# Performance work log

Measured on AMD Instinct MI355X. Metric: run time of the kernel, lower is better.

Reference implementation:

```python
import jax, jax.numpy as jnp
import numpy as np

NUM_BITS = 10
MEM_SIZE = 2 ** NUM_BITS  # 1024
HIDDEN = 1024
INPUT = 1024
BATCH = 16384
LN_EPS = 1e-5


def setup_inputs() -> dict:
    key = jax.random.key(0)
    ks = jax.random.split(key, 8)
    s = 0.02
    return {
        "x": jax.random.normal(ks[0], (BATCH, INPUT), jnp.float32),
        "h_prev": jax.random.normal(ks[1], (BATCH, HIDDEN), jnp.float32),
        "memory": jax.random.normal(ks[2], (MEM_SIZE, HIDDEN), jnp.float32),
        "W_w": jax.random.normal(ks[3], (HIDDEN, INPUT), jnp.float32) * s,
        "W_b": jnp.zeros((HIDDEN,), jnp.float32),
        "U_w": jax.random.normal(ks[4], (HIDDEN, HIDDEN), jnp.float32) * s,
        "U_b": jnp.zeros((HIDDEN,), jnp.float32),
        "Q_w": jax.random.normal(ks[5], (HIDDEN, HIDDEN), jnp.float32) * s,
        "Q_b": jnp.zeros((HIDDEN,), jnp.float32),
        "M_w": jax.random.normal(ks[6], (NUM_BITS, HIDDEN), jnp.float32) * s,
        "M_b": jnp.zeros((NUM_BITS,), jnp.float32),
        "ln_g": jnp.ones((HIDDEN,), jnp.float32),
        "ln_b": jnp.zeros((HIDDEN,), jnp.float32),
    }


def reference(x, h_prev, memory, W_w, W_b, U_w, U_b, Q_w, Q_b, M_w, M_b, ln_g, ln_b):
    # Binary address from h_prev (eval-mode hard threshold, non-differentiable)
    powers = jnp.asarray(2 ** np.arange(NUM_BITS - 1, -1, -1), dtype=x.dtype)  # [num_bits]
    logits = h_prev @ M_w.T + M_b                              # [B, num_bits]
    binary = (jax.nn.sigmoid(logits) > 0.5).astype(x.dtype)    # hard bits
    index = jnp.clip((binary * powers).sum(-1).astype(jnp.int32), 0, MEM_SIZE - 1)  # [B]
    h_mem = memory[index]                                      # gather [B, H]
    # Fused linear combine + LayerNorm + sigmoid
    pre = x @ W_w.T + W_b + h_prev @ U_w.T + U_b + h_mem @ Q_w.T + Q_b  # [B, H]
    mu = pre.mean(-1, keepdims=True)
    var = ((pre - mu) ** 2).mean(-1, keepdims=True)            # biased var (torch LN)
    norm = (pre - mu) * jax.lax.rsqrt(var + LN_EPS)
    return jax.nn.sigmoid(norm * ln_g + ln_b)                  # h_new [B, H]
```

## Files before the change

### kernel.cpp

```cpp
#include <hip/hip_runtime.h>

#define BATCH   16384
#define HIDDEN  1024
#define K2      2048
#define MEMSZ   1024
#define NBITS   10

#define BM 256
#define BN 256
#define BK 64
#define NT (K2 / BK)

typedef __bf16 bf16x8 __attribute__((ext_vector_type(8)));
typedef float  f32x4  __attribute__((ext_vector_type(4)));

__device__ __forceinline__ unsigned short f2bf(float f) {
    unsigned int u = __float_as_uint(f);
    u += 0x7FFFu + ((u >> 16) & 1u);
    return (unsigned short)(u >> 16);
}

__device__ __forceinline__ void gload_lds16(const void* g, void* l) {
    __builtin_amdgcn_global_load_lds(
        (const __attribute__((address_space(1))) unsigned int*)g,
        (__attribute__((address_space(3))) unsigned int*)l,
        16, 0, 0);
}

__global__ __launch_bounds__(256) void pack_build_kernel(
        const float* __restrict__ W, const float* __restrict__ U,
        const float* __restrict__ memory, const float* __restrict__ Q,
        const float* __restrict__ x, const float* __restrict__ h_prev,
        const float* __restrict__ M_w, const float* __restrict__ M_b,
        unsigned short* __restrict__ Bm, unsigned short* __restrict__ Mem,
        unsigned short* __restrict__ Qb, unsigned short* __restrict__ A,
        int* __restrict__ idxbuf) {
    if (blockIdx.x < 4096) {
        int u = blockIdx.x * 256 + threadIdx.x;
        const float* src;
        unsigned short* dst;
        if (u < 524288) {
            int n = u >> 9;
            int k = (u & 511) * 4;
            src = (k < 1024) ? (W + (size_t)n * 1024 + k)
                             : (U + (size_t)n * 1024 + (k - 1024));
            dst = Bm + (size_t)n * K2 + k;
        } else if (u < 786432) {
            int f = (u - 524288) * 4;
            src = memory + f;  dst = Mem + f;
        } else {
            int f = (u - 786432) * 4;
            src = Q + f;  dst = Qb + f;
        }
        float4 v = *reinterpret_cast<const float4*>(src);
        ushort4 o;
        o.x = f2bf(v.x); o.y = f2bf(v.y); o.z = f2bf(v.z); o.w = f2bf(v.w);
        *reinterpret_cast<ushort4*>(dst) = o;
        return;
    }

    int row  = ((blockIdx.x - 4096) * 256 + threadIdx.x) >> 6;
    int lane = threadIdx.x & 63;
    if (row >= BATCH) return;

    const float4* hp = reinterpret_cast<const float4*>(h_prev + (size_t)row * HIDDEN);
    float4 hv[4];
#pragma unroll
    for (int i = 0; i < 4; ++i) hv[i] = hp[i * 64 + lane];

    int idx = 0;
#pragma unroll
    for (int j = 0; j < NBITS; ++j) {
        const float4* mp = reinterpret_cast<const float4*>(M_w + (size_t)j * HIDDEN);
        float s = 0.f;
#pragma unroll
        for (int i = 0; i < 4; ++i) {
            float4 m = mp[i * 64 + lane];
            s += hv[i].x * m.x + hv[i].y * m.y + hv[i].z * m.z + hv[i].w * m.w;
        }
#pragma unroll
        for (int off = 32; off >= 1; off >>= 1) s += __shfl_xor(s, off, 64);
        float logit = s + M_b[j];
        if (logit > 0.f) idx |= (1 << (NBITS - 1 - j));
    }
    if (lane == 0) idxbuf[row] = idx;

    unsigned short* arow = A + (size_t)row * K2;
    const float4* xp = reinterpret_cast<const float4*>(x + (size_t)row * HIDDEN);
#pragma unroll
    for (int i = 0; i < 4; ++i) {
        int off = i * 256 + lane * 4;
        float4 vx = xp[i * 64 + lane];
        ushort4 ox; ox.x = f2bf(vx.x); ox.y = f2bf(vx.y); ox.z = f2bf(vx.z); ox.w = f2bf(vx.w);
        *reinterpret_cast<ushort4*>(arow + off) = ox;

        ushort4 oh; oh.x = f2bf(hv[i].x); oh.y = f2bf(hv[i].y); oh.z = f2bf(hv[i].z); oh.w = f2bf(hv[i].w);
        *reinterpret_cast<ushort4*>(arow + 1024 + off) = oh;
    }
}

__global__ __launch_bounds__(256) void mq_kernel(
        const unsigned short* __restrict__ Mem,
        const unsigned short* __restrict__ Qb,
        float* __restrict__ MQ) {
    __shared__ unsigned short As[128 * 64];
    __shared__ unsigned short Bs[128 * 64];

    const int ks = blockIdx.x >> 6;
    const int mb = (blockIdx.x >> 3) & 7;
    const int nb = blockIdx.x & 7;
    const int t    = threadIdx.x;
    const int lane = t & 63;
    const int w    = t >> 6;
    const int wr   = w >> 1, wc = w & 1;
    const int rr   = lane & 15, rq = lane >> 4;
    const int c8   = (t & 7) * 8;
    const int srow = t >> 3;

    f32x4 acc[4][4] = {};

    for (int kt = 0; kt < 4; ++kt) {
        const int k0 = ks * 256 + kt * 64;
#pragma unroll
        for (int i = 0; i < 4; ++i) {
            int r = i * 32 + srow;
            gload_lds16(Mem + (size_t)(mb * 128 + r) * 1024 + k0 + c8, As + i * 2048 + t * 8);
            gload_lds16(Qb  + (size_t)(nb * 128 + r) * 1024 + k0 + c8, Bs + i * 2048 + t * 8);
        }
        __syncthreads();
#pragma unroll
        for (int kk = 0; kk < 2; ++kk) {
            const int krd = kk * 32 + rq * 8;
            bf16x8 af[4], bfv[4];
#pragma unroll
            for (int m = 0; m < 4; ++m)
                af[m] = *reinterpret_cast<const bf16x8*>(As + (wr * 64 + m * 16 + rr) * 64 + krd);
#pragma unroll
            for (int n = 0; n < 4; ++n)
                bfv[n] = *reinterpret_cast<const bf16x8*>(Bs + (wc * 64 + n * 16 + rr) * 64 + krd);
#pragma unroll
            for (int m = 0; m < 4; ++m)
#pragma unroll
                for (int n = 0; n < 4; ++n)
                    acc[m][n] = __builtin_amdgcn_mfma_f32_16x16x32_bf16(
                        af[m], bfv[n], acc[m][n], 0, 0, 0);
        }
        __syncthreads();
    }

#pragma unroll
    for (int m = 0; m < 4; ++m)
#pragma unroll
        for (int n = 0; n < 4; ++n) {
            int gcol = nb * 128 + wc * 64 + n * 16 + rr;
#pragma unroll
            for (int j = 0; j < 4; ++j) {
                int grow = mb * 128 + wr * 64 + m * 16 + rq * 4 + j;
                atomicAdd(&MQ[(size_t)grow * 1024 + gcol], acc[m][n][j]);
            }
        }
}


__device__ __forceinline__ void stage_g(const unsigned short* __restrict__ src,
                                        int rowbase, int kt, int g,
                                        unsigned short* ldsTile, int t) {
    const int o      = g * 8192 + t * 16;
    const int row    = o >> 7;
    const int inner  = o & 127;
    const int sinner = inner ^ ((row & 7) << 4);
    const char* gp = reinterpret_cast<const char*>(
                         src + (size_t)(rowbase + row) * K2 + kt * BK) + sinner;
    gload_lds16(gp, reinterpret_cast<char*>(ldsTile) + o);
}

__device__ __forceinline__ bf16x8 ldsfrag(const unsigned short* tile, int row,
                                          int kbyte_x_sw) {
    return *reinterpret_cast<const bf16x8*>(
        reinterpret_cast<const char*>(tile) + row * 128 + kbyte_x_sw);
}

#define WAIT_PH(N)                                                   \
    do {                                                             \
        asm volatile("" ::: "memory");                               \
        __builtin_amdgcn_s_barrier();                                \
        asm volatile("s_waitcnt lgkmcnt(" #N ")" ::: "memory");      \
        __builtin_amdgcn_sched_barrier(0);                           \
    } while (0)

#define BAR_OUT()                                                    \
    do {                                                             \
        __builtin_amdgcn_sched_barrier(0);                           \
        asm volatile("" ::: "memory");                               \
        __builtin_amdgcn_s_barrier();                                \
    } while (0)

#define MFMA_Q(AF, BF, MB, NB)                                                 \
    {                                                                          \
        __builtin_amdgcn_s_setprio(1);                                         \
        _Pragma("unroll") for (int m_ = 0; m_ < 4; ++m_)                       \
        _Pragma("unroll") for (int n_ = 0; n_ < 2; ++n_)                       \
        _Pragma("unroll") for (int kk_ = 0; kk_ < 2; ++kk_)                    \
            acc[(MB) + m_][(NB) + n_] =                                        \
                __builtin_amdgcn_mfma_f32_16x16x32_bf16(                       \
                    AF[m_][kk_], BF[n_][kk_],                                  \
                    acc[(MB) + m_][(NB) + n_], 0, 0, 0);                       \
        __builtin_amdgcn_s_setprio(0);                                         \
    }

__global__ __launch_bounds__(512, 2) void gemm_kernel(
        const unsigned short* __restrict__ A,
        const unsigned short* __restrict__ Bm,
        float* __restrict__ C) {
    __shared__ alignas(16) unsigned short lds[2][2][BM * BK];

    const int bid  = blockIdx.x;
    const int wgid = (bid & 7) * 32 + (bid >> 3);
    const int mblk = wgid >> 2;
    const int nblk = wgid & 3;

    const int t    = threadIdx.x;
    const int lane = t & 63;
    const int w    = t >> 6;
    const int wr   = w >> 2;
    const int wc   = w & 3;
    const int rr   = lane & 15;
    const int rq   = lane >> 4;
    const int sw   = (rr & 7) << 4;
    const int rqb  = rq * 16;
    const int wrb  = wr * 128;
    const int wcb  = wc * 64;

    const int arow = mblk * BM;
    const int brow = nblk * BN;

    f32x4 acc[8][4] = {};

    {
#pragma unroll
        for (int g = 0; g < 4; ++g) stage_g(A,  arow, 0, g, &lds[0][0][0], t);
#pragma unroll
        for (int g = 0; g < 4; ++g) stage_g(Bm, brow, 0, g, &lds[0][1][0], t);
#pragma unroll
        for (int g = 0; g < 4; ++g) stage_g(Bm, brow, 1, g, &lds[1][1][0], t);
#pragma unroll
        for (int g = 0; g < 4; ++g) stage_g(A,  arow, 1, g, &lds[1][0][0], t);
        asm volatile("s_waitcnt vmcnt(8)" ::: "memory");
        asm volatile("" ::: "memory");
        __builtin_amdgcn_s_barrier();
    }

    bf16x8 af  [4][2];
    bf16x8 af2 [4][2];
    bf16x8 bfr01[2][2];
    bf16x8 bfr23[2][2];

#pragma unroll
    for (int m = 0; m < 4; ++m) {
        af[m][0] = ldsfrag(&lds[0][0][0], wrb + m * 16 + rr, (rqb) ^ sw);
        af[m][1] = ldsfrag(&lds[0][0][0], wrb + m * 16 + rr, (64 + rqb) ^ sw);
    }
#pragma unroll
    for (int n = 0; n < 2; ++n) {
        bfr01[n][0] = ldsfrag(&lds[0][1][0], wcb + n * 16 + rr, (rqb) ^ sw);
        bfr01[n][1] = ldsfrag(&lds[0][1][0], wcb + n * 16 + rr, (64 + rqb) ^ sw);
    }
    __builtin_amdgcn_sched_barrier(0);

    for (int kt = 0; kt < NT; ++kt) {
        const int c = kt & 1;
        const unsigned short* At  = &lds[c][0][0];
        const unsigned short* Bt  = &lds[c][1][0];
        const unsigned short* nxA = &lds[c ^ 1][0][0];
        const unsigned short* nxB = &lds[c ^ 1][1][0];
        unsigned short* curA = &lds[c][0][0];
        unsigned short* curB = &lds[c][1][0];
        const bool pf1 = (kt + 1 < NT);
        const bool pf2 = (kt + 2 < NT);

#pragma unroll
        for (int n = 0; n < 2; ++n) {
            bfr23[n][0] = ldsfrag(Bt, wcb + 32 + n * 16 + rr, (rqb) ^ sw);
            bfr23[n][1] = ldsfrag(Bt, wcb + 32 + n * 16 + rr, (64 + rqb) ^ sw);
        }
        __builtin_amdgcn_sched_barrier(0);
        af2[0][0] = ldsfrag(At, wrb + 64 + rr, (rqb) ^ sw);
        af2[0][1] = ldsfrag(At, wrb + 64 + rr, (64 + rqb) ^ sw);
        WAIT_PH(6);
        MFMA_Q(af, bfr01, 0, 0);
        BAR_OUT();

#pragma unroll
        for (int m = 1; m < 4; ++m) {
            af2[m][0] = ldsfrag(At, wrb + 64 + m * 16 + rr, (rqb) ^ sw);
            af2[m][1] = ldsfrag(At, wrb + 64 + m * 16 + rr, (64 + rqb) ^ sw);
        }
        WAIT_PH(8);
        MFMA_Q(af, bfr23, 0, 2);
        __builtin_amdgcn_sched_barrier(0);
        asm volatile("s_waitcnt vmcnt(0)" ::: "memory");
        asm volatile("" ::: "memory");
        __builtin_amdgcn_s_barrier();

        if (pf2) {
            stage_g(Bm, brow, kt + 2, 0, curB, t);
            stage_g(Bm, brow, kt + 2, 1, curB, t);
            stage_g(Bm, brow, kt + 2, 2, curB, t);
            stage_g(Bm, brow, kt + 2, 3, curB, t);
        }
        if (pf1) {
#pragma unroll
            for (int m = 0; m < 3; ++m) {
                af[m][0] = ldsfrag(nxA, wrb + m * 16 + rr, (rqb) ^ sw);
                af[m][1] = ldsfrag(nxA, wrb + m * 16 + rr, (64 + rqb) ^ sw);
            }
            WAIT_PH(6);
        } else {
            WAIT_PH(0);
        }
        MFMA_Q(af2, bfr01, 4, 0);
        BAR_OUT();

        if (pf2) {
            stage_g(A, arow, kt + 2, 0, curA, t);
            stage_g(A, arow, kt + 2, 1, curA, t);
            stage_g(A, arow, kt + 2, 2, curA, t);
            stage_g(A, arow, kt + 2, 3, curA, t);
        }
        if (pf1) {
            af[3][0] = ldsfrag(nxA, wrb + 48 + rr, (rqb) ^ sw);
            af[3][1] = ldsfrag(nxA, wrb + 48 + rr, (64 + rqb) ^ sw);
#pragma unroll
            for (int n = 0; n < 2; ++n) {
                bfr01[n][0] = ldsfrag(nxB, wcb + n * 16 + rr, (rqb) ^ sw);
                bfr01[n][1] = ldsfrag(nxB, wcb + n * 16 + rr, (64 + rqb) ^ sw);
            }
        }
        WAIT_PH(12);
        MFMA_Q(af2, bfr23, 4, 2);
        BAR_OUT();
    }

#pragma unroll
    for (int mi = 0; mi < 8; ++mi) {
#pragma unroll
        for (int n = 0; n < 4; ++n) {
            const int gcol = nblk * BN + wcb + n * 16 + rr;
#pragma unroll
            for (int j = 0; j < 4; ++j) {
                const int grow = mblk * BM + wrb + mi * 16 + rq * 4 + j;
                C[(size_t)grow * HIDDEN + gcol] = acc[mi][n][j];
            }
        }
    }
}

__global__ __launch_bounds__(256) void ln_kernel(
        float* __restrict__ C,
        const int* __restrict__ idxbuf,
        const float* __restrict__ MQ,
        const float* __restrict__ W_b, const float* __restrict__ U_b,
        const float* __restrict__ Q_b, const float* __restrict__ ln_g,
        const float* __restrict__ ln_b) {
    const int row = blockIdx.x;
    const int t   = threadIdx.x;
    const int midx = idxbuf[row];
    float4* rowp = reinterpret_cast<float4*>(C + (size_t)row * HIDDEN);
    const float4* mqp = reinterpret_cast<const float4*>(MQ + (size_t)midx * HIDDEN);

    float4 p  = rowp[t];
    float4 mq = mqp[t];
    float4 bw = reinterpret_cast<const float4*>(W_b)[t];
    float4 bu = reinterpret_cast<const float4*>(U_b)[t];
    float4 bq = reinterpret_cast<const float4*>(Q_b)[t];
    p.x += mq.x + bw.x + bu.x + bq.x;
    p.y += mq.y + bw.y + bu.y + bq.y;
    p.z += mq.z + bw.z + bu.z + bq.z;
    p.w += mq.w + bw.w + bu.w + bq.w;

    float s  = p.x + p.y + p.z + p.w;
    float sq = p.x * p.x + p.y * p.y + p.z * p.z + p.w * p.w;
#pragma unroll
    for (int off = 32; off >= 1; off >>= 1) {
        s  += __shfl_xor(s,  off, 64);
        sq += __shfl_xor(sq, off, 64);
    }
    __shared__ float red[8];
    const int lane = t & 63, w = t >> 6;
    if (lane == 0) { red[w] = s; red[4 + w] = sq; }
    __syncthreads();
    const float S    = red[0] + red[1] + red[2] + red[3];
    const float SQ   = red[4] + red[5] + red[6] + red[7];
    const float mean = S * (1.0f / HIDDEN);
    const float var  = SQ * (1.0f / HIDDEN) - mean * mean;
    const float rstd = rsqrtf(var + 1e-5f);

    float4 g = reinterpret_cast<const float4*>(ln_g)[t];
    float4 b = reinterpret_cast<const float4*>(ln_b)[t];
    float4 o;
    o.x = 1.f / (1.f + __expf(-((p.x - mean) * rstd * g.x + b.x)));
    o.y = 1.f / (1.f + __expf(-((p.y - mean) * rstd * g.y + b.y)));
    o.z = 1.f / (1.f + __expf(-((p.z - mean) * rstd * g.z + b.z)));
    o.w = 1.f / (1.f + __expf(-((p.w - mean) * rstd * g.w + b.w)));
    rowp[t] = o;
}

extern "C" void kernel_launch(void* const* d_in, const int* in_sizes, int n_in,
                              void* d_out, int out_size, void* d_ws, size_t ws_size,
                              hipStream_t stream) {
    const float* x      = (const float*)d_in[0];
    const float* h_prev = (const float*)d_in[1];
    const float* memory = (const float*)d_in[2];
    const float* W_w    = (const float*)d_in[3];
    const float* W_b    = (const float*)d_in[4];
    const float* U_w    = (const float*)d_in[5];
    const float* U_b    = (const float*)d_in[6];
    const float* Q_w    = (const float*)d_in[7];
    const float* Q_b    = (const float*)d_in[8];
    const float* M_w    = (const float*)d_in[9];
    const float* M_b    = (const float*)d_in[10];
    const float* ln_g   = (const float*)d_in[11];
    const float* ln_b   = (const float*)d_in[12];

    char* ws = (char*)d_ws;
    unsigned short* A   = (unsigned short*)(ws);
    unsigned short* Bm  = (unsigned short*)(ws + 67108864);
    unsigned short* Mem = (unsigned short*)(ws + 71303168);
    unsigned short* Qb  = (unsigned short*)(ws + 73400320);
    float*          MQ  = (float*)         (ws + 75497472);
    int*            idx = (int*)           (ws + 79691776);
    float* pre = (float*)d_out;

    hipLaunchKernelGGL(pack_build_kernel, dim3(8192), dim3(256), 0, stream,
                       W_w, U_w, memory, Q_w, x, h_prev, M_w, M_b,
                       Bm, Mem, Qb, A, idx);
    hipMemsetAsync(MQ, 0, (size_t)MEMSZ * HIDDEN * sizeof(float), stream);
    hipLaunchKernelGGL(mq_kernel, dim3(256), dim3(256), 0, stream,
                       Mem, Qb, MQ);
    hipLaunchKernelGGL(gemm_kernel, dim3((BATCH / BM) * (HIDDEN / BN)), dim3(512), 0, stream,
                       A, Bm, pre);
    hipLaunchKernelGGL(ln_kernel, dim3(BATCH), dim3(256), 0, stream,
                       pre, idx, MQ, W_b, U_b, Q_b, ln_g, ln_b);
}
```

Before: 166.6 us.

## Widen pack conversion to 8-wide, batch address-bit reductions, relax GEMM phase barriers

The pack kernel now converts 8 floats per thread with 16-byte bf16 stores, which halves its block count. The address computation loads h_prev and x up front, computes all ten partial dot products, then interleaves their shuffle reductions to expose more ILP than the serial per-bit reductions. The GEMM main loop moves each barrier to the start of its phase, drops the trailing barrier and the last lgkmcnt wait, and removes several sched_barriers so LDS reads can overlap MFMAs more freely. Fewer synchronisation points could introduce LDS read/write races if the reordered waits are not sufficient.

```diff
diff --git a/kernel.cpp b/kernel.cpp
--- a/kernel.cpp
+++ b/kernel.cpp
@@ -13,11 +13,19 @@
 
 typedef __bf16 bf16x8 __attribute__((ext_vector_type(8)));
 typedef float  f32x4  __attribute__((ext_vector_type(4)));
+typedef unsigned short u16x8 __attribute__((ext_vector_type(8)));
 
 __device__ __forceinline__ unsigned short f2bf(float f) {
     unsigned int u = __float_as_uint(f);
     u += 0x7FFFu + ((u >> 16) & 1u);
     return (unsigned short)(u >> 16);
+}
+
+__device__ __forceinline__ u16x8 f2bf8(float4 a, float4 b) {
+    u16x8 r;
+    r[0] = f2bf(a.x); r[1] = f2bf(a.y); r[2] = f2bf(a.z); r[3] = f2bf(a.w);
+    r[4] = f2bf(b.x); r[5] = f2bf(b.y); r[6] = f2bf(b.z); r[7] = f2bf(b.w);
+    return r;
 }
 
 __device__ __forceinline__ void gload_lds16(const void* g, void* l) {
@@ -35,68 +43,72 @@
         unsigned short* __restrict__ Bm, unsigned short* __restrict__ Mem,
         unsigned short* __restrict__ Qb, unsigned short* __restrict__ A,
         int* __restrict__ idxbuf) {
-    if (blockIdx.x < 4096) {
+    if (blockIdx.x < 2048) {
         int u = blockIdx.x * 256 + threadIdx.x;
         const float* src;
         unsigned short* dst;
-        if (u < 524288) {
-            int n = u >> 9;
-            int k = (u & 511) * 4;
-            src = (k < 1024) ? (W + (size_t)n * 1024 + k)
-                             : (U + (size_t)n * 1024 + (k - 1024));
-            dst = Bm + (size_t)n * K2 + k;
-        } else if (u < 786432) {
-            int f = (u - 524288) * 4;
+        if (u < 262144) {
+            int n  = u >> 8;
+            int k8 = (u & 255) << 3;
+            src = (k8 < 1024) ? (W + (size_t)n * 1024 + k8)
+                              : (U + (size_t)n * 1024 + (k8 - 1024));
+            dst = Bm + (size_t)n * K2 + k8;
+        } else if (u < 393216) {
+            int f = (u - 262144) << 3;
             src = memory + f;  dst = Mem + f;
         } else {
-            int f = (u - 786432) * 4;
+            int f = (u - 393216) << 3;
             src = Q + f;  dst = Qb + f;
         }
-        float4 v = *reinterpret_cast<const float4*>(src);
-        ushort4 o;
-        o.x = f2bf(v.x); o.y = f2bf(v.y); o.z = f2bf(v.z); o.w = f2bf(v.w);
-        *reinterpret_cast<ushort4*>(dst) = o;
+        float4 a = *reinterpret_cast<const float4*>(src);
+        float4 b = *reinterpret_cast<const float4*>(src + 4);
+        *reinterpret_cast<u16x8*>(dst) = f2bf8(a, b);
         return;
     }
 
-    int row  = ((blockIdx.x - 4096) * 256 + threadIdx.x) >> 6;
-    int lane = threadIdx.x & 63;
-    if (row >= BATCH) return;
-
-    const float4* hp = reinterpret_cast<const float4*>(h_prev + (size_t)row * HIDDEN);
-    float4 hv[4];
-#pragma unroll
-    for (int i = 0; i < 4; ++i) hv[i] = hp[i * 64 + lane];
-
+    const int row  = (blockIdx.x - 2048) * 4 + (threadIdx.x >> 6);
+    const int lane = threadIdx.x & 63;
+
+    const float* hr = h_prev + (size_t)row * HIDDEN;
+    const float* xr = x      + (size_t)row * HIDDEN;
+    float4 hA0 = *reinterpret_cast<const float4*>(hr + lane * 8);
+    float4 hA1 = *reinterpret_cast<const float4*>(hr + lane * 8 + 4);
+    float4 hB0 = *reinterpret_cast<const float4*>(hr + 512 + lane * 8);
+    float4 hB1 = *reinterpret_cast<const float4*>(hr + 512 + lane * 8 + 4);
+    float4 xA0 = *reinterpret_cast<const float4*>(xr + lane * 8);
+    float4 xA1 = *reinterpret_cast<const float4*>(xr + lane * 8 + 4);
+    float4 xB0 = *reinterpret_cast<const float4*>(xr + 512 + lane * 8);
+    float4 xB1 = *reinterpret_cast<const float4*>(xr + 512 + lane * 8 + 4);
+
+    float s[NBITS];
+#pragma unroll
+    for (int j = 0; j < NBITS; ++j) {
+        const float* mp = M_w + (size_t)j * HIDDEN;
+        float4 mA0 = *reinterpret_cast<const float4*>(mp + lane * 8);
+        float4 mA1 = *reinterpret_cast<const float4*>(mp + lane * 8 + 4);
+        float4 mB0 = *reinterpret_cast<const float4*>(mp + 512 + lane * 8);
+        float4 mB1 = *reinterpret_cast<const float4*>(mp + 512 + lane * 8 + 4);
+        s[j] = (hA0.x * mA0.x + hA0.y * mA0.y + hA0.z * mA0.z + hA0.w * mA0.w)
+             + (hA1.x * mA1.x + hA1.y * mA1.y + hA1.z * mA1.z + hA1.w * mA1.w)
+             + (hB0.x * mB0.x + hB0.y * mB0.y + hB0.z * mB0.z + hB0.w * mB0.w)
+             + (hB1.x * mB1.x + hB1.y * mB1.y + hB1.z * mB1.z + hB1.w * mB1.w);
+    }
+#pragma unroll
+    for (int off = 32; off >= 1; off >>= 1) {
+#pragma unroll
+        for (int j = 0; j < NBITS; ++j) s[j] += __shfl_xor(s[j], off, 64);
+    }
     int idx = 0;
 #pragma unroll
-    for (int j = 0; j < NBITS; ++j) {
-        const float4* mp = reinterpret_cast<const float4*>(M_w + (size_t)j * HIDDEN);
-        float s = 0.f;
-#pragma unroll
-        for (int i = 0; i < 4; ++i) {
-            float4 m = mp[i * 64 + lane];
-            s += hv[i].x * m.x + hv[i].y * m.y + hv[i].z * m.z + hv[i].w * m.w;
-        }
-#pragma unroll
-        for (int off = 32; off >= 1; off >>= 1) s += __shfl_xor(s, off, 64);
-        float logit = s + M_b[j];
-        if (logit > 0.f) idx |= (1 << (NBITS - 1 - j));
-    }
+    for (int j = 0; j < NBITS; ++j)
+        if (s[j] + M_b[j] > 0.f) idx |= 1 << (NBITS - 1 - j);
     if (lane == 0) idxbuf[row] = idx;
 
     unsigned short* arow = A + (size_t)row * K2;
-    const float4* xp = reinterpret_cast<const float4*>(x + (size_t)row * HIDDEN);
-#pragma unroll
-    for (int i = 0; i < 4; ++i) {
-        int off = i * 256 + lane * 4;
-        float4 vx = xp[i * 64 + lane];
-        ushort4 ox; ox.x = f2bf(vx.x); ox.y = f2bf(vx.y); ox.z = f2bf(vx.z); ox.w = f2bf(vx.w);
-        *reinterpret_cast<ushort4*>(arow + off) = ox;
-
-        ushort4 oh; oh.x = f2bf(hv[i].x); oh.y = f2bf(hv[i].y); oh.z = f2bf(hv[i].z); oh.w = f2bf(hv[i].w);
-        *reinterpret_cast<ushort4*>(arow + 1024 + off) = oh;
-    }
+    *reinterpret_cast<u16x8*>(arow + lane * 8)        = f2bf8(xA0, xA1);
+    *reinterpret_cast<u16x8*>(arow + 512 + lane * 8)  = f2bf8(xB0, xB1);
+    *reinterpret_cast<u16x8*>(arow + 1024 + lane * 8) = f2bf8(hA0, hA1);
+    *reinterpret_cast<u16x8*>(arow + 1536 + lane * 8) = f2bf8(hB0, hB1);
 }
 
 __global__ __launch_bounds__(256) void mq_kernel(
@@ -180,19 +192,17 @@
         reinterpret_cast<const char*>(tile) + row * 128 + kbyte_x_sw);
 }
 
-#define WAIT_PH(N)                                                   \
+#define PH_BAR()                                                     \
     do {                                                             \
         asm volatile("" ::: "memory");                               \
         __builtin_amdgcn_s_barrier();                                \
+        asm volatile("" ::: "memory");                               \
+    } while (0)
+
+#define LGKM(N)                                                      \
+    do {                                                             \
         asm volatile("s_waitcnt lgkmcnt(" #N ")" ::: "memory");      \
         __builtin_amdgcn_sched_barrier(0);                           \
-    } while (0)
-
-#define BAR_OUT()                                                    \
-    do {                                                             \
-        __builtin_amdgcn_sched_barrier(0);                           \
-        asm volatile("" ::: "memory");                               \
-        __builtin_amdgcn_s_barrier();                                \
     } while (0)
 
 #define MFMA_Q(AF, BF, MB, NB)                                                 \
@@ -265,7 +275,6 @@
         bfr01[n][0] = ldsfrag(&lds[0][1][0], wcb + n * 16 + rr, (rqb) ^ sw);
         bfr01[n][1] = ldsfrag(&lds[0][1][0], wcb + n * 16 + rr, (64 + rqb) ^ sw);
     }
-    __builtin_amdgcn_sched_barrier(0);
 
     for (int kt = 0; kt < NT; ++kt) {
         const int c = kt & 1;
@@ -278,30 +287,30 @@
         const bool pf1 = (kt + 1 < NT);
         const bool pf2 = (kt + 2 < NT);
 
+        PH_BAR();
 #pragma unroll
         for (int n = 0; n < 2; ++n) {
             bfr23[n][0] = ldsfrag(Bt, wcb + 32 + n * 16 + rr, (rqb) ^ sw);
             bfr23[n][1] = ldsfrag(Bt, wcb + 32 + n * 16 + rr, (64 + rqb) ^ sw);
         }
-        __builtin_amdgcn_sched_barrier(0);
         af2[0][0] = ldsfrag(At, wrb + 64 + rr, (rqb) ^ sw);
         af2[0][1] = ldsfrag(At, wrb + 64 + rr, (64 + rqb) ^ sw);
-        WAIT_PH(6);
+        LGKM(6);
         MFMA_Q(af, bfr01, 0, 0);
-        BAR_OUT();
-
+
+        PH_BAR();
 #pragma unroll
         for (int m = 1; m < 4; ++m) {
             af2[m][0] = ldsfrag(At, wrb + 64 + m * 16 + rr, (rqb) ^ sw);
             af2[m][1] = ldsfrag(At, wrb + 64 + m * 16 + rr, (64 + rqb) ^ sw);
         }
-        WAIT_PH(8);
+        LGKM(8);
         MFMA_Q(af, bfr23, 0, 2);
         __builtin_amdgcn_sched_barrier(0);
         asm volatile("s_waitcnt vmcnt(0)" ::: "memory");
         asm volatile("" ::: "memory");
-        __builtin_amdgcn_s_barrier();
-
+
+        PH_BAR();
         if (pf2) {
             stage_g(Bm, brow, kt + 2, 0, curB, t);
             stage_g(Bm, brow, kt + 2, 1, curB, t);
@@ -314,13 +323,13 @@
                 af[m][0] = ldsfrag(nxA, wrb + m * 16 + rr, (rqb) ^ sw);
                 af[m][1] = ldsfrag(nxA, wrb + m * 16 + rr, (64 + rqb) ^ sw);
             }
-            WAIT_PH(6);
+            LGKM(6);
         } else {
-            WAIT_PH(0);
+            LGKM(0);
         }
         MFMA_Q(af2, bfr01, 4, 0);
-        BAR_OUT();
-
+
+        PH_BAR();
         if (pf2) {
             stage_g(A, arow, kt + 2, 0, curA, t);
             stage_g(A, arow, kt + 2, 1, curA, t);
@@ -336,9 +345,7 @@
                 bfr01[n][1] = ldsfrag(nxB, wcb + n * 16 + rr, (64 + rqb) ^ sw);
             }
         }
-        WAIT_PH(12);
         MFMA_Q(af2, bfr23, 4, 2);
-        BAR_OUT();
     }
 
 #pragma unroll
@@ -431,7 +438,7 @@
     int*            idx = (int*)           (ws + 79691776);
     float* pre = (float*)d_out;
 
-    hipLaunchKernelGGL(pack_build_kernel, dim3(8192), dim3(256), 0, stream,
+    hipLaunchKernelGGL(pack_build_kernel, dim3(6144), dim3(256), 0, stream,
                        W_w, U_w, memory, Q_w, x, h_prev, M_w, M_b,
                        Bm, Mem, Qb, A, idx);
     hipMemsetAsync(MQ, 0, (size_t)MEMSZ * HIDDEN * sizeof(float), stream);
```

Result: slower. 171.2 us (+2.7%).
